# Performance work log

Hardware: AMD Instinct MI355X
Metric: run time of the kernel (lower is better)

Reference implementation:

```python
import jax, jax.numpy as jnp
import numpy as np

B, T, K = 512, 512, 64  # batch, seq_len, num_tags


def setup_inputs() -> dict:
    key = jax.random.key(0)
    k1, k2 = jax.random.split(key)
    inputs = jax.random.normal(k1, (B, T, K), dtype=jnp.float32)
    # learned CRF transition matrix (GlorotUniform-ish scale)
    transitions = jax.random.normal(k2, (K, K), dtype=jnp.float32) * 0.1
    return {"inputs": inputs, "transitions": transitions}


def _viterbi_decode(potentials, transitions, seq_lens):
    """Faithful jax version of tfa/tf crf_decode (max-plus Viterbi DP + backtrace).

    potentials: [B, T, K] unary scores
    transitions: [K, K] pairwise scores (from_tag, to_tag)
    seq_lens: [B] int valid lengths
    Returns (decode_tags [B, T] int32, best_score [B] float).
    """
    b, t, k = potentials.shape
    pots_t = jnp.transpose(potentials, (1, 0, 2))  # [T, B, K]
    # mask[t-1, b] = step t (1..T-1) is within sequence b
    mask = jnp.arange(1, t)[:, None] < seq_lens[None, :]  # [T-1, B]
    ident = jnp.arange(k, dtype=jnp.int32)

    def fwd_step(alpha, xs):
        pot_t, m = xs  # pot_t: [B, K], m: [B]
        scores = alpha[:, :, None] + transitions[None, :, :]  # [B, K_from, K_to]
        new_alpha = pot_t + jnp.max(scores, axis=1)           # [B, K]
        bp = jnp.argmax(scores, axis=1).astype(jnp.int32)     # [B, K]
        alpha = jnp.where(m[:, None], new_alpha, alpha)       # freeze past seq end
        bp = jnp.where(m[:, None], bp, ident[None, :])        # identity backptr
        return alpha, bp

    alpha0 = pots_t[0]
    alpha_final, bps = jax.lax.scan(fwd_step, alpha0, (pots_t[1:], mask))  # bps: [T-1, B, K]
    best_score = jnp.max(alpha_final, axis=1)                  # [B]
    last_tag = jnp.argmax(alpha_final, axis=1).astype(jnp.int32)  # [B]

    def back_step(tag, bp_t):
        prev = jnp.take_along_axis(bp_t, tag[:, None], axis=1)[:, 0]
        return prev, prev

    # reverse scan: ys[t] = best tag at time t, for t = 0..T-2
    _, prev_tags = jax.lax.scan(back_step, last_tag, bps, reverse=True)
    tags = jnp.concatenate([prev_tags, last_tag[None]], axis=0)  # [T, B]
    return jnp.transpose(tags), best_score


def reference(inputs, transitions):
    # sequence lengths derived exactly as in the original call()
    used = jnp.sign(jnp.abs(inputs))                       # [B, T, K]
    seq_lens = jnp.mean(jnp.sum(used, axis=1), axis=1)     # [B]
    seq_lens = seq_lens.astype(jnp.int32)
    decode_tags, _best_score = _viterbi_decode(inputs, transitions, seq_lens)
    return decode_tags
```

## Files before the change

kernel.cpp:

```cpp
#include <hip/hip_runtime.h>

#define BB 512
#define TT 512
#define KK 64

typedef float v2f __attribute__((ext_vector_type(2)));

__device__ __forceinline__ float frl(float v, int lane) {
    return __int_as_float(__builtin_amdgcn_readlane(__float_as_int(v), lane));
}
__device__ __forceinline__ v2f vmax2(v2f a, v2f b) {
    v2f r; r.x = fmaxf(a.x, b.x); r.y = fmaxf(a.y, b.y); return r;
}
__device__ __forceinline__ unsigned wave_umax63(unsigned x) {
    unsigned d;
    d = (unsigned)__builtin_amdgcn_update_dpp((int)x, (int)x, 0x111, 0xF, 0xF, false); x = x > d ? x : d;
    d = (unsigned)__builtin_amdgcn_update_dpp((int)x, (int)x, 0x112, 0xF, 0xF, false); x = x > d ? x : d;
    d = (unsigned)__builtin_amdgcn_update_dpp((int)x, (int)x, 0x114, 0xF, 0xF, false); x = x > d ? x : d;
    d = (unsigned)__builtin_amdgcn_update_dpp((int)x, (int)x, 0x118, 0xF, 0xF, false); x = x > d ? x : d;
    d = (unsigned)__builtin_amdgcn_update_dpp((int)x, (int)x, 0x142, 0xA, 0xF, false); x = x > d ? x : d;
    d = (unsigned)__builtin_amdgcn_update_dpp((int)x, (int)x, 0x143, 0xC, 0xF, false); x = x > d ? x : d;
    return x;
}

#define FSTEP(PT, TC) do {                                                      \
    la[lane] = alpha;                                                           \
    asm volatile("" ::: "memory");                                              \
    v2f acc0, acc1, acc2, acc3;                                                 \
    {                                                                           \
        float4 a4 = ((float4*)la)[0];                                           \
        v2f lo; lo.x = a4.x; lo.y = a4.y; acc0 = lo + tcl[0];                   \
        v2f hi; hi.x = a4.z; hi.y = a4.w; acc1 = hi + tch[0];                   \
        a4 = ((float4*)la)[1];                                                  \
        lo.x = a4.x; lo.y = a4.y; acc2 = lo + tcl[1];                           \
        hi.x = a4.z; hi.y = a4.w; acc3 = hi + tch[1];                           \
    }                                                                           \
    _Pragma("unroll")                                                           \
    for (int c = 2; c < 16; c += 2) {                                           \
        float4 a4 = ((float4*)la)[c];                                           \
        v2f lo; lo.x = a4.x; lo.y = a4.y; acc0 = vmax2(acc0, lo + tcl[c]);      \
        v2f hi; hi.x = a4.z; hi.y = a4.w; acc1 = vmax2(acc1, hi + tch[c]);      \
        a4 = ((float4*)la)[c + 1];                                              \
        lo.x = a4.x; lo.y = a4.y; acc2 = vmax2(acc2, lo + tcl[c + 1]);          \
        hi.x = a4.z; hi.y = a4.w; acc3 = vmax2(acc3, hi + tch[c + 1]);          \
    }                                                                           \
    v2f mm = vmax2(vmax2(acc0, acc1), vmax2(acc2, acc3));                       \
    float M = fmaxf(mm.x, mm.y);                                                \
    alpha = (TC) ? (PT + M) : alpha;                                            \
    *hp = alpha; hp += KK;                                                      \
} while (0)

__global__ __launch_bounds__(64, 1) void crf_fused(const float* __restrict__ pot,
                                                   const float* __restrict__ trans,
                                                   float* __restrict__ alphaH,
                                                   int* __restrict__ out) {
    __shared__ float tT[KK][KK + 1];
    __shared__ float la[KK];

    const int b = blockIdx.x;
    const int lane = threadIdx.x;
    const float* pb = pot + (size_t)b * TT * KK;
    float* hb = alphaH + (size_t)b * TT * KK;
    int* ob = out + b * TT;

    int cnt = 0;
    {
        const float4* p4 = (const float4*)pb;
        #pragma unroll 4
        for (int r = 0; r < 128; ++r) {
            float4 v = p4[lane + 64 * r];
            cnt += (v.x != 0.f) + (v.y != 0.f) + (v.z != 0.f) + (v.w != 0.f);
        }
        #pragma unroll
        for (int off = 32; off > 0; off >>= 1) cnt += __shfl_xor(cnt, off, 64);
    }
    const int seqlen = cnt >> 6;

    #pragma unroll 8
    for (int r = 0; r < KK; ++r) tT[lane][r] = trans[r * KK + lane];

    v2f tcl[16], tch[16];
    #pragma unroll
    for (int c = 0; c < 16; ++c) {
        v2f l2, h2;
        l2.x = trans[(4 * c + 0) * KK + lane]; l2.y = trans[(4 * c + 1) * KK + lane];
        h2.x = trans[(4 * c + 2) * KK + lane]; h2.y = trans[(4 * c + 3) * KK + lane];
        tcl[c] = l2; tch[c] = h2;
    }
    #pragma unroll
    for (int c = 0; c < 16; ++c) {
        asm volatile("" : "+v"(tcl[c]));
        asm volatile("" : "+v"(tch[c]));
    }

    float alpha = pb[lane];
    hb[lane] = alpha;
    float* hp = hb + KK + lane;

    float pf[4] = { pb[1 * KK + lane], pb[2 * KK + lane], pb[3 * KK + lane], pb[4 * KK + lane] };
    const float* lp = pb + 5 * KK + lane;

    int t = 1;
    #pragma unroll 1
    for (int c = 0; c < 126; ++c) {
        #pragma unroll
        for (int u = 0; u < 4; ++u) {
            FSTEP(pf[u], t < seqlen);
            pf[u] = *lp; lp += KK;
            ++t;
        }
    }
    float e0 = pb[509 * KK + lane], e1 = pb[510 * KK + lane], e2 = pb[511 * KK + lane];
    FSTEP(pf[0], 505 < seqlen);
    FSTEP(pf[1], 506 < seqlen);
    FSTEP(pf[2], 507 < seqlen);
    FSTEP(pf[3], 508 < seqlen);
    FSTEP(e0, 509 < seqlen);
    FSTEP(e1, 510 < seqlen);
    FSTEP(e2, 511 < seqlen);

    asm volatile("s_waitcnt vmcnt(0)" ::: "memory");

    float v = alpha; int idx = lane;
    #pragma unroll
    for (int off = 1; off < 64; off <<= 1) {
        float vo = __shfl_xor(v, off, 64);
        int io = __shfl_xor(idx, off, 64);
        bool take = (vo > v) || (vo == v && io < idx);
        v = take ? vo : v;
        idx = take ? io : idx;
    }
    int cur = idx;
    int slot = cur;

    float r0 = hb[510 * KK + lane], r1 = hb[509 * KK + lane], r2 = hb[508 * KK + lane],
          r3 = hb[507 * KK + lane], r4 = hb[506 * KK + lane], r5 = hb[505 * KK + lane],
          r6 = hb[504 * KK + lane], r7 = hb[503 * KK + lane];

    auto bt_step = [&](int tt, float arow) {
        if (tt < seqlen) {
            float cand = arow + tT[cur][lane];
            unsigned u = __float_as_uint(cand);
            u = u ^ ((unsigned)(((int)u) >> 31) | 0x80000000u);
            unsigned run = wave_umax63(u);
            unsigned Umax = (unsigned)__builtin_amdgcn_readlane((int)run, 63);
            unsigned long long mk = __ballot(u == Umax);
            cur = (int)__builtin_ctzll(mk);
        }
        const int tm = tt - 1;
        slot = ((tm & 63) == lane) ? cur : slot;
        if ((tm & 63) == 0) ob[tm + lane] = slot;
    };

    int T0 = 511;
    for (int c = 0; c < 63; ++c) {
        bt_step(T0 - 0, r0); { int pi = T0 - 9;  pi = pi < 0 ? 0 : pi; r0 = hb[pi * KK + lane]; }
        bt_step(T0 - 1, r1); { int pi = T0 - 10; pi = pi < 0 ? 0 : pi; r1 = hb[pi * KK + lane]; }
        bt_step(T0 - 2, r2); { int pi = T0 - 11; pi = pi < 0 ? 0 : pi; r2 = hb[pi * KK + lane]; }
        bt_step(T0 - 3, r3); { int pi = T0 - 12; pi = pi < 0 ? 0 : pi; r3 = hb[pi * KK + lane]; }
        bt_step(T0 - 4, r4); { int pi = T0 - 13; pi = pi < 0 ? 0 : pi; r4 = hb[pi * KK + lane]; }
        bt_step(T0 - 5, r5); { int pi = T0 - 14; pi = pi < 0 ? 0 : pi; r5 = hb[pi * KK + lane]; }
        bt_step(T0 - 6, r6); { int pi = T0 - 15; pi = pi < 0 ? 0 : pi; r6 = hb[pi * KK + lane]; }
        bt_step(T0 - 7, r7); { int pi = T0 - 16; pi = pi < 0 ? 0 : pi; r7 = hb[pi * KK + lane]; }
        T0 -= 8;
    }
    bt_step(7, r0); bt_step(6, r1); bt_step(5, r2); bt_step(4, r3);
    bt_step(3, r4); bt_step(2, r5); bt_step(1, r6);
}

__global__ __launch_bounds__(256) void seqlen_kernel(const float* __restrict__ inp,
                                                     int* __restrict__ seq_lens) {
    int b = blockIdx.x;
    int tid = threadIdx.x;
    const float4* p4 = (const float4*)(inp + (size_t)b * TT * KK);
    const int n4 = TT * KK / 4;
    int cnt = 0;
    for (int idx = tid; idx < n4; idx += 256) {
        float4 v = p4[idx];
        cnt += (v.x != 0.0f) + (v.y != 0.0f) + (v.z != 0.0f) + (v.w != 0.0f);
    }
    #pragma unroll
    for (int off = 32; off > 0; off >>= 1) cnt += __shfl_down(cnt, off, 64);
    __shared__ int wsum[4];
    if ((tid & 63) == 0) wsum[tid >> 6] = cnt;
    __syncthreads();
    if (tid == 0) seq_lens[b] = (wsum[0] + wsum[1] + wsum[2] + wsum[3]) >> 6;
}

__global__ __launch_bounds__(64) void viterbi_fallback(const float* __restrict__ pot,
                                                       const float* __restrict__ trans,
                                                       const int* __restrict__ seq_lens,
                                                       int* __restrict__ out) {
    __shared__ unsigned char bp[TT][KK];
    const int b = blockIdx.x;
    const int j = threadIdx.x;

    float tc[KK];
    #pragma unroll
    for (int i = 0; i < KK; ++i) tc[i] = trans[i * KK + j];

    const float* pb = pot + (size_t)b * TT * KK;
    float alpha = pb[j];
    const int seqlen = seq_lens[b];

    for (int t = 1; t < TT; ++t) {
        float ptj = pb[t * KK + j];
        float m[4]; int am[4];
        #pragma unroll
        for (int c = 0; c < 4; ++c) {
            const int i = c * 16;
            float ai = frl(alpha, i);
            m[c] = ai + tc[i];
            am[c] = i;
        }
        #pragma unroll
        for (int q = 1; q < 16; ++q) {
            #pragma unroll
            for (int c = 0; c < 4; ++c) {
                const int i = c * 16 + q;
                float ai = frl(alpha, i);
                float s = ai + tc[i];
                bool g = s > m[c];
                m[c] = g ? s : m[c];
                am[c] = g ? i : am[c];
            }
        }
        float M = m[0]; int BI = am[0];
        #pragma unroll
        for (int c = 1; c < 4; ++c) {
            bool g = m[c] > M;
            M = g ? m[c] : M;
            BI = g ? am[c] : BI;
        }
        const bool valid = (t < seqlen);
        alpha = valid ? (ptj + M) : alpha;
        bp[t][j] = (unsigned char)(valid ? BI : j);
    }

    float v = alpha; int idx = j;
    #pragma unroll
    for (int off = 1; off < 64; off <<= 1) {
        float vo = __shfl_xor(v, off, 64);
        int io = __shfl_xor(idx, off, 64);
        bool take = (vo > v) || (vo == v && io < idx);
        v = take ? vo : v;
        idx = take ? io : idx;
    }
    __syncthreads();
    if (j == 0) {
        int* ob = out + b * TT;
        int cur = idx;
        ob[TT - 1] = cur;
        for (int p = TT - 2; p >= 0; --p) {
            cur = bp[p + 1][cur];
            ob[p] = cur;
        }
    }
}

extern "C" void kernel_launch(void* const* d_in, const int* in_sizes, int n_in,
                              void* d_out, int out_size, void* d_ws, size_t ws_size,
                              hipStream_t stream) {
    const float* inp = (const float*)d_in[0];
    const float* trans = (const float*)d_in[1];
    int* out = (int*)d_out;

    const size_t histBytes = (size_t)BB * TT * KK * sizeof(float);
    if (ws_size >= histBytes) {
        float* alphaH = (float*)d_ws;
        crf_fused<<<BB, 64, 0, stream>>>(inp, trans, alphaH, out);
    } else {
        int* seq = (int*)d_ws;
        seqlen_kernel<<<BB, 256, 0, stream>>>(inp, seq);
        viterbi_fallback<<<BB, KK, 0, stream>>>(inp, trans, seq, out);
    }
}
```

Before: 283.1 us.

## Store per-step max instead of alpha and recover backpointers by equality match

The forward recurrence now runs for all steps without the seqlen mask and stores the per-step max M rather than alpha. The final alpha for shorter sequences is reconstructed from the potentials plus the stored max. The seqlen count moves after the forward loop so the nonzero scan no longer sits in front of the serial recurrence. Backtrace replaces the DPP wave-max argmax with a ballot on equality against the stored max read from the current tag's lane. The forward inner reduction uses v_max3_f32 to cut instruction count. The risk is exactness: the equality match depends on bitwise identical recomputation of p + M + trans and falls back to keeping the old tag if nothing matches.

```diff
diff --git a/kernel.cpp b/kernel.cpp
--- a/kernel.cpp
+++ b/kernel.cpp
@@ -9,45 +9,40 @@
 __device__ __forceinline__ float frl(float v, int lane) {
     return __int_as_float(__builtin_amdgcn_readlane(__float_as_int(v), lane));
 }
-__device__ __forceinline__ v2f vmax2(v2f a, v2f b) {
-    v2f r; r.x = fmaxf(a.x, b.x); r.y = fmaxf(a.y, b.y); return r;
-}
-__device__ __forceinline__ unsigned wave_umax63(unsigned x) {
-    unsigned d;
-    d = (unsigned)__builtin_amdgcn_update_dpp((int)x, (int)x, 0x111, 0xF, 0xF, false); x = x > d ? x : d;
-    d = (unsigned)__builtin_amdgcn_update_dpp((int)x, (int)x, 0x112, 0xF, 0xF, false); x = x > d ? x : d;
-    d = (unsigned)__builtin_amdgcn_update_dpp((int)x, (int)x, 0x114, 0xF, 0xF, false); x = x > d ? x : d;
-    d = (unsigned)__builtin_amdgcn_update_dpp((int)x, (int)x, 0x118, 0xF, 0xF, false); x = x > d ? x : d;
-    d = (unsigned)__builtin_amdgcn_update_dpp((int)x, (int)x, 0x142, 0xA, 0xF, false); x = x > d ? x : d;
-    d = (unsigned)__builtin_amdgcn_update_dpp((int)x, (int)x, 0x143, 0xC, 0xF, false); x = x > d ? x : d;
-    return x;
-}
-
-#define FSTEP(PT, TC) do {                                                      \
+__device__ __forceinline__ float fmax3(float a, float b, float c) {
+    float d;
+    asm("v_max3_f32 %0, %1, %2, %3" : "=v"(d) : "v"(a), "v"(b), "v"(c));
+    return d;
+}
+
+#define FSTEP(PT) do {                                                          \
     la[lane] = alpha;                                                           \
     asm volatile("" ::: "memory");                                              \
-    v2f acc0, acc1, acc2, acc3;                                                 \
+    float acc0, acc1, acc2, acc3;                                               \
     {                                                                           \
         float4 a4 = ((float4*)la)[0];                                           \
-        v2f lo; lo.x = a4.x; lo.y = a4.y; acc0 = lo + tcl[0];                   \
-        v2f hi; hi.x = a4.z; hi.y = a4.w; acc1 = hi + tch[0];                   \
+        v2f lo; lo.x = a4.x; lo.y = a4.y; v2f cl = lo + tcl[0];                 \
+        v2f hi; hi.x = a4.z; hi.y = a4.w; v2f ch = hi + tch[0];                 \
+        acc0 = fmaxf(cl.x, cl.y); acc1 = fmaxf(ch.x, ch.y);                     \
         a4 = ((float4*)la)[1];                                                  \
-        lo.x = a4.x; lo.y = a4.y; acc2 = lo + tcl[1];                           \
-        hi.x = a4.z; hi.y = a4.w; acc3 = hi + tch[1];                           \
+        lo.x = a4.x; lo.y = a4.y; cl = lo + tcl[1];                             \
+        hi.x = a4.z; hi.y = a4.w; ch = hi + tch[1];                             \
+        acc2 = fmaxf(cl.x, cl.y); acc3 = fmaxf(ch.x, ch.y);                     \
     }                                                                           \
     _Pragma("unroll")                                                           \
     for (int c = 2; c < 16; c += 2) {                                           \
         float4 a4 = ((float4*)la)[c];                                           \
-        v2f lo; lo.x = a4.x; lo.y = a4.y; acc0 = vmax2(acc0, lo + tcl[c]);      \
-        v2f hi; hi.x = a4.z; hi.y = a4.w; acc1 = vmax2(acc1, hi + tch[c]);      \
+        v2f lo; lo.x = a4.x; lo.y = a4.y; v2f cl = lo + tcl[c];                 \
+        v2f hi; hi.x = a4.z; hi.y = a4.w; v2f ch = hi + tch[c];                 \
+        acc0 = fmax3(acc0, cl.x, cl.y); acc1 = fmax3(acc1, ch.x, ch.y);         \
         a4 = ((float4*)la)[c + 1];                                              \
-        lo.x = a4.x; lo.y = a4.y; acc2 = vmax2(acc2, lo + tcl[c + 1]);          \
-        hi.x = a4.z; hi.y = a4.w; acc3 = vmax2(acc3, hi + tch[c + 1]);          \
+        lo.x = a4.x; lo.y = a4.y; cl = lo + tcl[c + 1];                         \
+        hi.x = a4.z; hi.y = a4.w; ch = hi + tch[c + 1];                         \
+        acc2 = fmax3(acc2, cl.x, cl.y); acc3 = fmax3(acc3, ch.x, ch.y);         \
     }                                                                           \
-    v2f mm = vmax2(vmax2(acc0, acc1), vmax2(acc2, acc3));                       \
-    float M = fmaxf(mm.x, mm.y);                                                \
-    alpha = (TC) ? (PT + M) : alpha;                                            \
-    *hp = alpha; hp += KK;                                                      \
+    float M = fmaxf(fmax3(acc0, acc1, acc2), acc3);                             \
+    *hp = M; hp += KK;                                                          \
+    alpha = (PT) + M;                                                           \
 } while (0)
 
 __global__ __launch_bounds__(64, 1) void crf_fused(const float* __restrict__ pot,
@@ -62,6 +57,42 @@
     const float* pb = pot + (size_t)b * TT * KK;
     float* hb = alphaH + (size_t)b * TT * KK;
     int* ob = out + b * TT;
+
+    #pragma unroll 8
+    for (int r = 0; r < KK; ++r) tT[lane][r] = trans[r * KK + lane];
+
+    v2f tcl[16], tch[16];
+    #pragma unroll
+    for (int c = 0; c < 16; ++c) {
+        v2f l2, h2;
+        l2.x = trans[(4 * c + 0) * KK + lane]; l2.y = trans[(4 * c + 1) * KK + lane];
+        h2.x = trans[(4 * c + 2) * KK + lane]; h2.y = trans[(4 * c + 3) * KK + lane];
+        tcl[c] = l2; tch[c] = h2;
+    }
+    #pragma unroll
+    for (int c = 0; c < 16; ++c) {
+        asm volatile("" : "+v"(tcl[c]));
+        asm volatile("" : "+v"(tch[c]));
+    }
+
+    float alpha = pb[lane];
+    hb[lane] = 0.0f;
+    float* hp = hb + KK + lane;
+
+    float pf[4] = { pb[1 * KK + lane], pb[2 * KK + lane], pb[3 * KK + lane], pb[4 * KK + lane] };
+    const float* lp = pb + 5 * KK + lane;
+
+    #pragma unroll 1
+    for (int c = 0; c < 126; ++c) {
+        #pragma unroll
+        for (int u = 0; u < 4; ++u) {
+            FSTEP(pf[u]);
+            pf[u] = *lp; lp += KK;
+        }
+    }
+    float e0 = pb[509 * KK + lane], e1 = pb[510 * KK + lane], e2 = pb[511 * KK + lane];
+    FSTEP(pf[0]); FSTEP(pf[1]); FSTEP(pf[2]); FSTEP(pf[3]);
+    FSTEP(e0);    FSTEP(e1);    FSTEP(e2);
 
     int cnt = 0;
     {
@@ -76,52 +107,15 @@
     }
     const int seqlen = cnt >> 6;
 
-    #pragma unroll 8
-    for (int r = 0; r < KK; ++r) tT[lane][r] = trans[r * KK + lane];
-
-    v2f tcl[16], tch[16];
-    #pragma unroll
-    for (int c = 0; c < 16; ++c) {
-        v2f l2, h2;
-        l2.x = trans[(4 * c + 0) * KK + lane]; l2.y = trans[(4 * c + 1) * KK + lane];
-        h2.x = trans[(4 * c + 2) * KK + lane]; h2.y = trans[(4 * c + 3) * KK + lane];
-        tcl[c] = l2; tch[c] = h2;
-    }
-    #pragma unroll
-    for (int c = 0; c < 16; ++c) {
-        asm volatile("" : "+v"(tcl[c]));
-        asm volatile("" : "+v"(tch[c]));
-    }
-
-    float alpha = pb[lane];
-    hb[lane] = alpha;
-    float* hp = hb + KK + lane;
-
-    float pf[4] = { pb[1 * KK + lane], pb[2 * KK + lane], pb[3 * KK + lane], pb[4 * KK + lane] };
-    const float* lp = pb + 5 * KK + lane;
-
-    int t = 1;
-    #pragma unroll 1
-    for (int c = 0; c < 126; ++c) {
-        #pragma unroll
-        for (int u = 0; u < 4; ++u) {
-            FSTEP(pf[u], t < seqlen);
-            pf[u] = *lp; lp += KK;
-            ++t;
-        }
-    }
-    float e0 = pb[509 * KK + lane], e1 = pb[510 * KK + lane], e2 = pb[511 * KK + lane];
-    FSTEP(pf[0], 505 < seqlen);
-    FSTEP(pf[1], 506 < seqlen);
-    FSTEP(pf[2], 507 < seqlen);
-    FSTEP(pf[3], 508 < seqlen);
-    FSTEP(e0, 509 < seqlen);
-    FSTEP(e1, 510 < seqlen);
-    FSTEP(e2, 511 < seqlen);
-
     asm volatile("s_waitcnt vmcnt(0)" ::: "memory");
 
-    float v = alpha; int idx = lane;
+    float afin = alpha;
+    if (seqlen < TT) {
+        if (seqlen <= 1) afin = pb[lane];
+        else afin = pb[(seqlen - 1) * KK + lane] + hb[(seqlen - 1) * KK + lane];
+    }
+
+    float v = afin; int idx = lane;
     #pragma unroll
     for (int off = 1; off < 64; off <<= 1) {
         float vo = __shfl_xor(v, off, 64);
@@ -133,39 +127,42 @@
     int cur = idx;
     int slot = cur;
 
-    float r0 = hb[510 * KK + lane], r1 = hb[509 * KK + lane], r2 = hb[508 * KK + lane],
-          r3 = hb[507 * KK + lane], r4 = hb[506 * KK + lane], r5 = hb[505 * KK + lane],
-          r6 = hb[504 * KK + lane], r7 = hb[503 * KK + lane];
-
-    auto bt_step = [&](int tt, float arow) {
+    float mrow = hb[511 * KK + lane];
+    float m0 = hb[510 * KK + lane], m1 = hb[509 * KK + lane], m2 = hb[508 * KK + lane],
+          m3 = hb[507 * KK + lane], m4 = hb[506 * KK + lane], m5 = hb[505 * KK + lane],
+          m6 = hb[504 * KK + lane], m7 = hb[503 * KK + lane];
+    float p0 = pb[510 * KK + lane], p1 = pb[509 * KK + lane], p2 = pb[508 * KK + lane],
+          p3 = pb[507 * KK + lane], p4 = pb[506 * KK + lane], p5 = pb[505 * KK + lane],
+          p6 = pb[504 * KK + lane], p7 = pb[503 * KK + lane];
+
+    auto bt_step = [&](int tt, float mlo, float plo) {
         if (tt < seqlen) {
-            float cand = arow + tT[cur][lane];
-            unsigned u = __float_as_uint(cand);
-            u = u ^ ((unsigned)(((int)u) >> 31) | 0x80000000u);
-            unsigned run = wave_umax63(u);
-            unsigned Umax = (unsigned)__builtin_amdgcn_readlane((int)run, 63);
-            unsigned long long mk = __ballot(u == Umax);
-            cur = (int)__builtin_ctzll(mk);
-        }
+            float target = frl(mrow, cur);
+            float cand = (plo + mlo) + tT[cur][lane];
+            unsigned long long mk = __ballot(cand == target);
+            if (mk) cur = (int)__builtin_ctzll(mk);
+        }
+        mrow = mlo;
         const int tm = tt - 1;
         slot = ((tm & 63) == lane) ? cur : slot;
         if ((tm & 63) == 0) ob[tm + lane] = slot;
     };
 
     int T0 = 511;
+    #pragma unroll 1
     for (int c = 0; c < 63; ++c) {
-        bt_step(T0 - 0, r0); { int pi = T0 - 9;  pi = pi < 0 ? 0 : pi; r0 = hb[pi * KK + lane]; }
-        bt_step(T0 - 1, r1); { int pi = T0 - 10; pi = pi < 0 ? 0 : pi; r1 = hb[pi * KK + lane]; }
-        bt_step(T0 - 2, r2); { int pi = T0 - 11; pi = pi < 0 ? 0 : pi; r2 = hb[pi * KK + lane]; }
-        bt_step(T0 - 3, r3); { int pi = T0 - 12; pi = pi < 0 ? 0 : pi; r3 = hb[pi * KK + lane]; }
-        bt_step(T0 - 4, r4); { int pi = T0 - 13; pi = pi < 0 ? 0 : pi; r4 = hb[pi * KK + lane]; }
-        bt_step(T0 - 5, r5); { int pi = T0 - 14; pi = pi < 0 ? 0 : pi; r5 = hb[pi * KK + lane]; }
-        bt_step(T0 - 6, r6); { int pi = T0 - 15; pi = pi < 0 ? 0 : pi; r6 = hb[pi * KK + lane]; }
-        bt_step(T0 - 7, r7); { int pi = T0 - 16; pi = pi < 0 ? 0 : pi; r7 = hb[pi * KK + lane]; }
+        bt_step(T0 - 0, m0, p0); { int pi = T0 - 9;  pi = pi < 0 ? 0 : pi; m0 = hb[pi * KK + lane]; p0 = pb[pi * KK + lane]; }
+        bt_step(T0 - 1, m1, p1); { int pi = T0 - 10; pi = pi < 0 ? 0 : pi; m1 = hb[pi * KK + lane]; p1 = pb[pi * KK + lane]; }
+        bt_step(T0 - 2, m2, p2); { int pi = T0 - 11; pi = pi < 0 ? 0 : pi; m2 = hb[pi * KK + lane]; p2 = pb[pi * KK + lane]; }
+        bt_step(T0 - 3, m3, p3); { int pi = T0 - 12; pi = pi < 0 ? 0 : pi; m3 = hb[pi * KK + lane]; p3 = pb[pi * KK + lane]; }
+        bt_step(T0 - 4, m4, p4); { int pi = T0 - 13; pi = pi < 0 ? 0 : pi; m4 = hb[pi * KK + lane]; p4 = pb[pi * KK + lane]; }
+        bt_step(T0 - 5, m5, p5); { int pi = T0 - 14; pi = pi < 0 ? 0 : pi; m5 = hb[pi * KK + lane]; p5 = pb[pi * KK + lane]; }
+        bt_step(T0 - 6, m6, p6); { int pi = T0 - 15; pi = pi < 0 ? 0 : pi; m6 = hb[pi * KK + lane]; p6 = pb[pi * KK + lane]; }
+        bt_step(T0 - 7, m7, p7); { int pi = T0 - 16; pi = pi < 0 ? 0 : pi; m7 = hb[pi * KK + lane]; p7 = pb[pi * KK + lane]; }
         T0 -= 8;
     }
-    bt_step(7, r0); bt_step(6, r1); bt_step(5, r2); bt_step(4, r3);
-    bt_step(3, r4); bt_step(2, r5); bt_step(1, r6);
+    bt_step(7, m0, p0); bt_step(6, m1, p1); bt_step(5, m2, p2); bt_step(4, m3, p3);
+    bt_step(3, m4, p4); bt_step(2, m5, p5); bt_step(1, m6, p6);
 }
 
 __global__ __launch_bounds__(256) void seqlen_kernel(const float* __restrict__ inp,
```

Result: faster. 259.5 us (-8.3%).
